# Optimization experiments

Measured on AMD Instinct MI355X. Metric: run time of the kernel, lower is better.

Reference implementation:

```python
import jax, jax.numpy as jnp
import numpy as np

B, H, C, HID, WIN, K = 8, 64, 128, 512, 4, 3
L = H * H

def _conv(x, w, groups, pad):
    return jax.lax.conv_general_dilated(
        x, w, (1, 1), [(pad, pad), (pad, pad)],
        dimension_numbers=('NCHW', 'OIHW', 'NCHW'), feature_group_count=groups)

def _ln(x, g, b):
    m = x.mean(-1, keepdims=True)
    v = ((x - m) ** 2).mean(-1, keepdims=True)
    return (x - m) * jax.lax.rsqrt(v + 1e-5) * g + b

def _gelu(x):
    return jax.nn.gelu(x, approximate=False)  # torch nn.GELU default = erf

def setup_inputs() -> dict:
    key = jax.random.key(0)
    ks = jax.random.split(key, 16)
    n = lambda i, sh: jax.random.normal(ks[i], sh, jnp.float32) * 0.02
    return dict(
        x=jax.random.normal(ks[0], (B, L, C), jnp.float32),
        ln1_g=jnp.ones((C,), jnp.float32), ln1_b=jnp.zeros((C,), jnp.float32),
        conv1_w=n(1, (WIN * C, C, K, K)),
        w_down=n(2, (WIN, C)), b_down=jnp.zeros((WIN,), jnp.float32),
        w1=n(3, (4 * WIN, WIN)), b1=jnp.zeros((4 * WIN,), jnp.float32),
        w2=n(4, (WIN, 4 * WIN)), b2=jnp.zeros((WIN,), jnp.float32),
        w_gk=n(5, (C, WIN * C)), b_gk=jnp.zeros((C,), jnp.float32),
        w_fus=n(6, (C, (WIN + 1) * C)), b_fus=jnp.zeros((C,), jnp.float32),
        ln2_g=jnp.ones((C,), jnp.float32), ln2_b=jnp.zeros((C,), jnp.float32),
        lin1_w=n(7, (HID, C)), lin1_b=jnp.zeros((HID,), jnp.float32),
        dw_w=n(8, (HID, 1, K, K)), dw_b=jnp.zeros((HID,), jnp.float32),
        lin2_w=n(9, (C, HID)), lin2_b=jnp.zeros((C,), jnp.float32),
    )

def _kernel_attn(x, conv1_w, w_down, b_down, w1, b1, w2, b2, w_gk, b_gk, w_fus, b_fus):
    ws = H // 2  # window grid is 2x2 since win_num=4
    xw = x.reshape(B, 2, ws, 2, ws, C).transpose(0, 1, 3, 5, 2, 4).reshape(B, WIN * C, ws, ws)
    wc = _conv(xw, conv1_w, WIN, 1)
    # WinKernel_Reweight (SE over windows)
    pooled = wc.mean((2, 3)).reshape(B, WIN, C)
    y = jnp.einsum('bgc,gc->bg', pooled, w_down) + b_down
    y = _gelu(y @ w1.T + b1)
    wgt = jax.nn.sigmoid(y @ w2.T + b2)
    k0 = conv1_w.reshape(WIN, C, C, K, K)
    kern = wgt[:, :, None, None, None, None] * k0[None]
    k_in = kern.transpose(0, 2, 1, 3, 4, 5).reshape(B * C, WIN * C, K, K)
    gk = jnp.einsum('om,nmij->noij', w_gk, k_in) + b_gk[None, :, None, None]
    kernels = jnp.concatenate([kern, gk.reshape(B, 1, C, C, K, K)], axis=1)
    kernels = kernels.reshape(B * (WIN + 1) * C, C, K, K)
    # per-sample dynamic grouped conv over full-resolution image
    ximg = x.reshape(B, H, H, C).transpose(0, 3, 1, 2)     # [B, C, H, W]
    xrep = jnp.tile(ximg, (1, WIN + 1, 1, 1)).reshape(1, B * (WIN + 1) * C, H, H)
    out = _conv(xrep, kernels, B * (WIN + 1), 1).reshape(B, (WIN + 1) * C, H, H)
    out = jnp.einsum('oc,bchw->bohw', w_fus, out) + b_fus[None, :, None, None]
    return out.transpose(0, 2, 3, 1).reshape(B, L, C)

def _leff(x, lin1_w, lin1_b, dw_w, dw_b, lin2_w, lin2_b):
    h = _gelu(x @ lin1_w.T + lin1_b)                       # [B, L, HID]
    h = h.reshape(B, H, H, HID).transpose(0, 3, 1, 2)
    h = _gelu(_conv(h, dw_w, HID, 1) + dw_b[None, :, None, None])  # depthwise 3x3
    h = h.transpose(0, 2, 3, 1).reshape(B, L, HID)
    return h @ lin2_w.T + lin2_b

def reference(x, ln1_g, ln1_b, conv1_w, w_down, b_down, w1, b1, w2, b2,
              w_gk, b_gk, w_fus, b_fus, ln2_g, ln2_b,
              lin1_w, lin1_b, dw_w, dw_b, lin2_w, lin2_b):
    x = x + _kernel_attn(_ln(x, ln1_g, ln1_b), conv1_w, w_down, b_down,
                         w1, b1, w2, b2, w_gk, b_gk, w_fus, b_fus)
    x = x + _leff(_ln(x, ln2_g, ln2_b), lin1_w, lin1_b, dw_w, dw_b, lin2_w, lin2_b)
    return x
```

## Files before the change

kernel.cpp:

```cpp
#include <hip/hip_runtime.h>
#include <math.h>

#define NB   8
#define HH   64
#define NC   128
#define NHID 512
#define NL   4096

typedef __attribute__((ext_vector_type(4))) float f32x4;
typedef __attribute__((ext_vector_type(8))) __bf16 bf16x8;

__device__ __forceinline__ float gelu_f(float v) {
  return 0.5f * v * (1.f + erff(v * 0.70710678118654752f));
}
__device__ __forceinline__ float sigmoid_f(float v) {
  return 1.f / (1.f + expf(-v));
}
__device__ __forceinline__ unsigned short f2bf(float f) {
  unsigned int u = __builtin_bit_cast(unsigned int, f);
  unsigned int r = (u + 0x7FFFu + ((u >> 16) & 1u)) >> 16;
  return (unsigned short)r;
}
__device__ __forceinline__ float bf2f(unsigned short h) {
  return __builtin_bit_cast(float, ((unsigned int)h) << 16);
}
__device__ __forceinline__ float bflo(unsigned int w) {
  return __builtin_bit_cast(float, w << 16);
}
__device__ __forceinline__ float bfhi(unsigned int w) {
  return __builtin_bit_cast(float, w & 0xFFFF0000u);
}
__device__ __forceinline__ void gld16(const void* g, void* l) {
  __builtin_amdgcn_global_load_lds(
      (const __attribute__((address_space(1))) unsigned int*)g,
      (__attribute__((address_space(3))) unsigned int*)l, 16, 0, 0);
}

template<bool SWZ>
__global__ __launch_bounds__(256) void ln_kernel(const float* __restrict__ x,
    const float* __restrict__ g, const float* __restrict__ bb, unsigned short* __restrict__ out) {
  int wv = threadIdx.x >> 6, l = threadIdx.x & 63;
  int row = blockIdx.x * 4 + wv;
  const float2 v = *(const float2*)(x + (size_t)row * NC + l * 2);
  float s = v.x + v.y, ss = v.x * v.x + v.y * v.y;
#pragma unroll
  for (int off = 32; off > 0; off >>= 1) {
    s  += __shfl_down(s, off);
    ss += __shfl_down(ss, off);
  }
  s = __shfl(s, 0); ss = __shfl(ss, 0);
  float mean = s * (1.f / NC);
  float rstd = rsqrtf(ss * (1.f / NC) - mean * mean + 1e-5f);
  const float2 gg = *(const float2*)(g + l * 2);
  const float2 bv = *(const float2*)(bb + l * 2);
  float o0 = (v.x - mean) * rstd * gg.x + bv.x;
  float o1 = (v.y - mean) * rstd * gg.y + bv.y;
  unsigned int pk = (unsigned int)f2bf(o0) | ((unsigned int)f2bf(o1) << 16);
  int c16 = l >> 2;
  int cs = SWZ ? (c16 ^ (row & 7)) : c16;
  *(unsigned int*)((char*)out + (size_t)row * 256 + (cs << 4) + (l & 3) * 4) = pk;
}

__global__ __launch_bounds__(128) void rs_kernel(const unsigned short* __restrict__ xln,
    float* __restrict__ RS) {
  int blk = blockIdx.x;
  int r = blk & 31, bw = blk >> 5;
  int win = bw & 3, b = bw >> 2;
  int hw = win >> 1, wn = win & 1;
  int cin = threadIdx.x;
  const unsigned short* base = xln + (((size_t)(b * 64 + hw * 32 + r)) * 64 + wn * 32) * NC + cin;
  float s = 0;
#pragma unroll
  for (int c = 0; c < 32; ++c) s += bf2f(base[(size_t)c * NC]);
  RS[(size_t)blk * 128 + cin] = s;
}

__global__ __launch_bounds__(128) void tfin_kernel(const unsigned short* __restrict__ xln,
    const float* __restrict__ RS, float* __restrict__ T) {
  int bw = blockIdx.x;
  int win = bw & 3, b = bw >> 2;
  int hw = win >> 1, wn = win & 1;
  int cin = threadIdx.x;
  const unsigned short* base = xln + (((size_t)(b * 64 + hw * 32)) * 64 + wn * 32) * NC + cin;
  float A = 0;
#pragma unroll
  for (int r = 0; r < 32; ++r) A += RS[(size_t)(bw * 32 + r) * 128 + cin];
  float r0  = RS[(size_t)(bw * 32) * 128 + cin];
  float r31 = RS[(size_t)(bw * 32 + 31) * 128 + cin];
  float c0 = 0, c31 = 0;
#pragma unroll
  for (int r = 0; r < 32; ++r) {
    c0  += bf2f(base[((size_t)r * 64) * NC]);
    c31 += bf2f(base[((size_t)r * 64 + 31) * NC]);
  }
  float x00 = bf2f(base[0]);
  float x0c = bf2f(base[(size_t)31 * NC]);
  float xr0 = bf2f(base[((size_t)31 * 64) * NC]);
  float xrc = bf2f(base[((size_t)31 * 64 + 31) * NC]);
  float* t = T + ((size_t)bw * 128 + cin) * 9;
  t[0] = A - r31 - c31 + xrc;
  t[1] = A - r31;
  t[2] = A - r31 - c0 + xr0;
  t[3] = A - c31;
  t[4] = A;
  t[5] = A - c0;
  t[6] = A - r0 - c31 + x0c;
  t[7] = A - r0;
  t[8] = A - r0 - c0 + x00;
}

__global__ __launch_bounds__(256) void se_kernel(const float* __restrict__ T,
    const float* __restrict__ U, const float* __restrict__ b_down,
    const float* __restrict__ w1, const float* __restrict__ b1,
    const float* __restrict__ w2, const float* __restrict__ b2, float* __restrict__ wgt) {
  __shared__ float ydot[32];
  int tid = threadIdx.x;
  int pair = tid >> 3, sub = tid & 7;
  int g = pair & 3;
  float acc = 0;
  const float* up = U + (size_t)g * 1152 + sub * 144;
  const float* tp = T + (size_t)pair * 1152 + sub * 144;
  for (int i = 0; i < 144; ++i) acc += up[i] * tp[i];
#pragma unroll
  for (int off = 4; off > 0; off >>= 1) acc += __shfl_down(acc, off);
  if (sub == 0) ydot[pair] = acc;
  __syncthreads();
  if (tid < NB) {
    int b = tid;
    float y[4];
#pragma unroll
    for (int gg = 0; gg < 4; ++gg) y[gg] = ydot[b * 4 + gg] * (1.f / 1024.f) + b_down[gg];
    float y1[16];
#pragma unroll
    for (int i = 0; i < 16; ++i) {
      float a = b1[i];
#pragma unroll
      for (int gg = 0; gg < 4; ++gg) a += y[gg] * w1[i * 4 + gg];
      y1[i] = gelu_f(a);
    }
#pragma unroll
    for (int gg = 0; gg < 4; ++gg) {
      float a = b2[gg];
#pragma unroll
      for (int i = 0; i < 16; ++i) a += y1[i] * w2[gg * 16 + i];
      wgt[b * 4 + gg] = sigmoid_f(a);
    }
  }
}

__global__ __launch_bounds__(128) void prep_ct_kernel(const float* __restrict__ conv1_w,
    unsigned short* __restrict__ ctp, unsigned short* __restrict__ ctq) {
  int oc = blockIdx.x;
  int w = oc >> 7, c = oc & 127;
  int t = threadIdx.x;
  float v[9];
#pragma unroll
  for (int j = 0; j < 9; ++j) v[j] = conv1_w[(size_t)oc * 1152 + t * 9 + j];
#pragma unroll
  for (int j = 0; j < 9; ++j) {
    unsigned short bv = f2bf(v[j]);
    size_t prow = (size_t)(w * 9 + j) * 128 + c;
    *(unsigned short*)((char*)ctp + prow * 256 + ((((t >> 3) ^ (c & 7)) << 4) + (t & 7) * 2)) = bv;
    size_t qrow = (size_t)(w * 9 + j) * 128 + t;
    *(unsigned short*)((char*)ctq + qrow * 256 + ((((c >> 3) ^ (t & 7)) << 4) + (c & 7) * 2)) = bv;
  }
}

__global__ __launch_bounds__(256) void prep_misc_kernel(
    const float* __restrict__ lin1_w, const float* __restrict__ lin2_w,
    const float* __restrict__ w_gk, const float* __restrict__ w_fus,
    const float* __restrict__ dw_w, const float* __restrict__ conv1_w,
    const float* __restrict__ w_down,
    unsigned short* __restrict__ w1o, unsigned short* __restrict__ w2o,
    unsigned short* __restrict__ wgko, unsigned short* __restrict__ wf1o,
    unsigned short* __restrict__ wf2o, float* __restrict__ dwt,
    float* __restrict__ U, float* __restrict__ sfus) {
  int blk = blockIdx.x, tid = threadIdx.x;
  if (blk < 32) {
    int idx = blk * 256 + tid;
    int n = idx >> 4, c16 = idx & 15;
    const float4 a = *(const float4*)(lin1_w + (size_t)n * 128 + c16 * 8);
    const float4 b = *(const float4*)(lin1_w + (size_t)n * 128 + c16 * 8 + 4);
    unsigned int p0 = (unsigned int)f2bf(a.x) | ((unsigned int)f2bf(a.y) << 16);
    unsigned int p1 = (unsigned int)f2bf(a.z) | ((unsigned int)f2bf(a.w) << 16);
    unsigned int p2 = (unsigned int)f2bf(b.x) | ((unsigned int)f2bf(b.y) << 16);
    unsigned int p3 = (unsigned int)f2bf(b.z) | ((unsigned int)f2bf(b.w) << 16);
    *(uint4*)((char*)w1o + (size_t)n * 256 + ((c16 ^ (n & 7)) << 4)) = make_uint4(p0, p1, p2, p3);
  } else if (blk < 64) {
    int idx = (blk - 32) * 256 + tid;
    int kt = idx >> 11, c = (idx >> 4) & 127, c16 = idx & 15;
    const float* s = lin2_w + (size_t)c * NHID + kt * 128 + c16 * 8;
    const float4 a = *(const float4*)(s);
    const float4 b = *(const float4*)(s + 4);
    unsigned int p0 = (unsigned int)f2bf(a.x) | ((unsigned int)f2bf(a.y) << 16);
    unsigned int p1 = (unsigned int)f2bf(a.z) | ((unsigned int)f2bf(a.w) << 16);
    unsigned int p2 = (unsigned int)f2bf(b.x) | ((unsigned int)f2bf(b.y) << 16);
    unsigned int p3 = (unsigned int)f2bf(b.z) | ((unsigned int)f2bf(b.w) << 16);
    *(uint4*)((char*)w2o + (size_t)(kt * 128 + c) * 256 + ((c16 ^ (c & 7)) << 4)) = make_uint4(p0, p1, p2, p3);
  } else if (blk < 96) {
    int idx = (blk - 64) * 256 + tid;
    int row = idx >> 4, c16 = idx & 15;
    int w = row >> 7, q = row & 127;
    const float* s = w_gk + (size_t)q * 512 + w * 128 + c16 * 8;
    const float4 a = *(const float4*)(s);
    const float4 b = *(const float4*)(s + 4);
    unsigned int p0 = (unsigned int)f2bf(a.x) | ((unsigned int)f2bf(a.y) << 16);
    unsigned int p1 = (unsigned int)f2bf(a.z) | ((unsigned int)f2bf(a.w) << 16);
    unsigned int p2 = (unsigned int)f2bf(b.x) | ((unsigned int)f2bf(b.y) << 16);
    unsigned int p3 = (unsigned int)f2bf(b.z) | ((unsigned int)f2bf(b.w) << 16);
    *(uint4*)((char*)wgko + (size_t)row * 256 + ((c16 ^ (row & 7)) << 4)) = make_uint4(p0, p1, p2, p3);
  } else if (blk < 136) {
    int idx = (blk - 96) * 256 + tid;
    if (idx < 8192) {
      int row = idx >> 4, c16 = idx & 15;
      int w = row >> 7, o = row & 127;
      const float* s = w_fus + (size_t)o * 640 + w * 128 + c16 * 8;
      const float4 a = *(const float4*)(s);
      const float4 b = *(const float4*)(s + 4);
      unsigned int p0 = (unsigned int)f2bf(a.x) | ((unsigned int)f2bf(a.y) << 16);
      unsigned int p1 = (unsigned int)f2bf(a.z) | ((unsigned int)f2bf(a.w) << 16);
      unsigned int p2 = (unsigned int)f2bf(b.x) | ((unsigned int)f2bf(b.y) << 16);
      unsigned int p3 = (unsigned int)f2bf(b.z) | ((unsigned int)f2bf(b.w) << 16);
      *(uint4*)((char*)wf1o + (size_t)row * 256 + ((c16 ^ (row & 7)) << 4)) = make_uint4(p0, p1, p2, p3);
    } else if (idx < 10240) {
      int i2 = idx - 8192;
      int row = i2 >> 4, c16 = i2 & 15;
      const float* s = w_fus + (size_t)row * 640 + 512 + c16 * 8;
      const float4 a = *(const float4*)(s);
      const float4 b = *(const float4*)(s + 4);
      unsigned int p0 = (unsigned int)f2bf(a.x) | ((unsigned int)f2bf(a.y) << 16);
      unsigned int p1 = (unsigned int)f2bf(a.z) | ((unsigned int)f2bf(a.w) << 16);
      unsigned int p2 = (unsigned int)f2bf(b.x) | ((unsigned int)f2bf(b.y) << 16);
      unsigned int p3 = (unsigned int)f2bf(b.z) | ((unsigned int)f2bf(b.w) << 16);
      *(uint4*)((char*)wf2o + (size_t)row * 256 + ((c16 ^ (row & 7)) << 4)) = make_uint4(p0, p1, p2, p3);
    }
  } else if (blk < 154) {
    int idx = (blk - 136) * 256 + tid;
    if (idx < 4608) {
      int p = idx / 1152, rem = idx - p * 1152;
      int tap = rem >> 7, c = rem & 127;
      dwt[idx] = dw_w[(size_t)(p * 128 + c) * 9 + tap];
    }
  } else if (blk < 172) {
    int idx = (blk - 154) * 256 + tid;
    if (idx < 4608) {
      int g = idx / 1152, rem = idx - g * 1152;
      float s = 0;
      for (int cout = 0; cout < 128; ++cout)
        s += w_down[g * 128 + cout] * conv1_w[(size_t)(g * 128 + cout) * 1152 + rem];
      U[idx] = s;
    }
  } else {
    if (tid < 128) {
      float s = 0;
      for (int p = 0; p < 128; ++p) s += w_fus[(size_t)tid * 640 + 512 + p];
      sfus[tid] = s;
    }
  }
}

__global__ __launch_bounds__(256) void gemmG_kernel(const unsigned short* __restrict__ Wgk,
    const unsigned short* __restrict__ CTP, unsigned short* __restrict__ Gbf) {
  __shared__ uint4 LA[2048];
  __shared__ uint4 LB[2048];
  int bx = blockIdx.x;
  int w = bx / 9;
  int tid = threadIdx.x, wv = tid >> 6, l = tid & 63;
  const char* ga = (const char*)Wgk + (size_t)w * 32768;
  const char* gb = (const char*)CTP + (size_t)bx * 32768;
  for (int i = wv; i < 32; i += 4) gld16(ga + (i << 10) + l * 16, (char*)LA + (i << 10));
  for (int i = wv; i < 32; i += 4) gld16(gb + (i << 10) + l * 16, (char*)LB + (i << 10));
  __syncthreads();
  const f32x4 zero = {0.f, 0.f, 0.f, 0.f};
  f32x4 acc[2][8];
#pragma unroll
  for (int mt = 0; mt < 2; ++mt)
#pragma unroll
    for (int nt = 0; nt < 8; ++nt) acc[mt][nt] = zero;
  bf16x8 af[2][4];
#pragma unroll
  for (int mt = 0; mt < 2; ++mt) {
    int r = wv * 16 + mt * 64 + (l & 15);
#pragma unroll
    for (int ks = 0; ks < 4; ++ks) {
      int c16 = ks * 4 + (l >> 4);
      af[mt][ks] = *(const bf16x8*)((const char*)LA + r * 256 + ((c16 ^ (r & 7)) << 4));
    }
  }
#pragma unroll
  for (int nt = 0; nt < 8; ++nt) {
    int n = nt * 16 + (l & 15);
    bf16x8 bq[4];
#pragma unroll
    for (int ks = 0; ks < 4; ++ks) {
      int c16 = ks * 4 + (l >> 4);
      bq[ks] = *(const bf16x8*)((const char*)LB + n * 256 + ((c16 ^ (n & 7)) << 4));
    }
#pragma unroll
    for (int ks = 0; ks < 4; ++ks)
#pragma unroll
      for (int mt = 0; mt < 2; ++mt)
        acc[mt][nt] = __builtin_amdgcn_mfma_f32_16x16x32_bf16(af[mt][ks], bq[ks], acc[mt][nt], 0, 0, 0);
  }
  char* gout = (char*)Gbf + (size_t)bx * 32768;
#pragma unroll
  for (int mt = 0; mt < 2; ++mt)
#pragma unroll
    for (int nt = 0; nt < 8; ++nt) {
      int p = nt * 16 + (l & 15);
#pragma unroll
      for (int r2 = 0; r2 < 4; ++r2) {
        int q = wv * 16 + mt * 64 + (l >> 4) * 4 + r2;
        *(unsigned short*)(gout + q * 256 + ((((p >> 3) ^ (q & 7)) << 4) + (p & 7) * 2)) =
            f2bf(acc[mt][nt][r2]);
      }
    }
}

__global__ __launch_bounds__(256) void gemmAW_kernel(const unsigned short* __restrict__ Wf1,
    const unsigned short* __restrict__ CTQ, const unsigned short* __restrict__ Wf2,
    const unsigned short* __restrict__ Gbf, float* __restrict__ AW) {
  __shared__ uint4 LA[2048];
  __shared__ uint4 LB[2048];
  int bx = blockIdx.x;
  int w = bx / 9;
  int tid = threadIdx.x, wv = tid >> 6, l = tid & 63;
  const f32x4 zero = {0.f, 0.f, 0.f, 0.f};
  f32x4 acc[2][8];
#pragma unroll
  for (int mt = 0; mt < 2; ++mt)
#pragma unroll
    for (int nt = 0; nt < 8; ++nt) acc[mt][nt] = zero;
  for (int ph = 0; ph < 2; ++ph) {
    if (ph) __syncthreads();
    const char* ga = ph ? (const char*)Wf2 : (const char*)Wf1 + (size_t)w * 32768;
    const char* gb = ph ? (const char*)Gbf + (size_t)bx * 32768
                        : (const char*)CTQ + (size_t)bx * 32768;
    for (int i = wv; i < 32; i += 4) gld16(ga + (i << 10) + l * 16, (char*)LA + (i << 10));
    for (int i = wv; i < 32; i += 4) gld16(gb + (i << 10) + l * 16, (char*)LB + (i << 10));
    __syncthreads();
    bf16x8 af[2][4];
#pragma unroll
    for (int mt = 0; mt < 2; ++mt) {
      int r = wv * 16 + mt * 64 + (l & 15);
#pragma unroll
      for (int ks = 0; ks < 4; ++ks) {
        int c16 = ks * 4 + (l >> 4);
        af[mt][ks] = *(const bf16x8*)((const char*)LA + r * 256 + ((c16 ^ (r & 7)) << 4));
      }
    }
#pragma unroll
    for (int nt = 0; nt < 8; ++nt) {
      int n = nt * 16 + (l & 15);
      bf16x8 bq[4];
#pragma unroll
      for (int ks = 0; ks < 4; ++ks) {
        int c16 = ks * 4 + (l >> 4);
        bq[ks] = *(const bf16x8*)((const char*)LB + n * 256 + ((c16 ^ (n & 7)) << 4));
      }
#pragma unroll
      for (int ks = 0; ks < 4; ++ks)
#pragma unroll
        for (int mt = 0; mt < 2; ++mt)
          acc[mt][nt] = __builtin_amdgcn_mfma_f32_16x16x32_bf16(af[mt][ks], bq[ks], acc[mt][nt], 0, 0, 0);
    }
  }
  float* aout = AW + (size_t)bx * 16384;
#pragma unroll
  for (int mt = 0; mt < 2; ++mt)
#pragma unroll
    for (int nt = 0; nt < 8; ++nt) {
      int q = nt * 16 + (l & 15);
#pragma unroll
      for (int r2 = 0; r2 < 4; ++r2) {
        int o = wv * 16 + mt * 64 + (l >> 4) * 4 + r2;
        aout[(size_t)o * 128 + q] = acc[mt][nt][r2];
      }
    }
}

__global__ __launch_bounds__(128) void m_kernel(const float* __restrict__ AW,
    const float* __restrict__ wgt, const float* __restrict__ sfus,
    const float* __restrict__ b_gk, unsigned short* __restrict__ Mb) {
  int blk = blockIdx.x;
  int b = blk >> 7;
  int o = blk & 127;
  int q = threadIdx.x;
  float a3 = sfus[o] * b_gk[q];
  float acc[9];
#pragma unroll
  for (int ij = 0; ij < 9; ++ij) acc[ij] = a3;
#pragma unroll
  for (int w = 0; w < 4; ++w) {
    float wv = wgt[b * 4 + w];
#pragma unroll
    for (int ij = 0; ij < 9; ++ij)
      acc[ij] += wv * AW[(((size_t)(w * 9 + ij) * 128 + o) * 128) + q];
  }
  int qswz = (q & 7) | (((q >> 3) ^ (o & 7)) << 3);
#pragma unroll
  for (int ij = 0; ij < 9; ++ij)
    Mb[(((size_t)(b * 9 + ij) * NC + o) * NC) + qswz] = f2bf(acc[ij]);
}

__global__ __launch_bounds__(256) void conv_kernel(const float* __restrict__ x0,
    const unsigned short* __restrict__ xln, const unsigned short* __restrict__ Mb,
    const float* __restrict__ b_fus, const float* __restrict__ ln2g,
    const float* __restrict__ ln2b, float* __restrict__ xout,
    unsigned short* __restrict__ xln2) {
  __shared__ uint4 XT[1600];
  __shared__ uint4 MT[2048];
  int bx = blockIdx.x;
  int b = bx >> 6, tile = bx & 63;
  int by = (tile >> 3) * 8, bxc = (tile & 7) * 8;
  int tid = threadIdx.x, wv = tid >> 6, l = tid & 63;
  for (int i = tid; i < 1600; i += 256) {
    int cell = i >> 4, c16 = i & 15;
    int pr = cell / 10, pc = cell - pr * 10;
    int gy = by + pr - 1, gx = bxc + pc - 1;
    uint4 v = make_uint4(0, 0, 0, 0);
    if ((unsigned)gy < 64u && (unsigned)gx < 64u)
      v = *(const uint4*)(xln + (((size_t)b * NL + gy * 64 + gx) * NC + c16 * 8));
    *(uint4*)((char*)XT + cell * 256 + ((c16 ^ (cell & 7)) << 4)) = v;
  }
  const char* mg = (const char*)Mb + (size_t)b * 9 * 32768;
  for (int i = wv; i < 32; i += 4) gld16(mg + (i << 10) + l * 16, (char*)MT + (i << 10));
  __syncthreads();

  const f32x4 zero = {0.f, 0.f, 0.f, 0.f};
  f32x4 acc[8];
#pragma unroll
  for (int nt = 0; nt < 8; ++nt) acc[nt] = zero;

  int sp = wv * 16 + (l & 15);
  int srow = sp >> 3, scol = sp & 7;

  for (int ij = 0; ij < 9; ++ij) {
    int di = ij / 3, dj = ij - di * 3;
    int cell = (srow + di) * 10 + scol + dj;
    bf16x8 af[4];
#pragma unroll
    for (int ks = 0; ks < 4; ++ks) {
      int c16 = ks * 4 + (l >> 4);
      af[ks] = *(const bf16x8*)((const char*)XT + cell * 256 + ((c16 ^ (cell & 7)) << 4));
    }
#pragma unroll
    for (int nt = 0; nt < 8; ++nt) {
      int oc = nt * 16 + (l & 15);
      bf16x8 bq[4];
#pragma unroll
      for (int ks = 0; ks < 4; ++ks) {
        int c16 = ks * 4 + (l >> 4);
        bq[ks] = *(const bf16x8*)((const char*)MT + oc * 256 + ((c16 ^ (oc & 7)) << 4));
      }
#pragma unroll
      for (int ks = 0; ks < 4; ++ks)
        acc[nt] = __builtin_amdgcn_mfma_f32_16x16x32_bf16(af[ks], bq[ks], acc[nt], 0, 0, 0);
    }
    __syncthreads();
    if (ij < 8) {
      const char* mg2 = mg + (size_t)(ij + 1) * 32768;
      for (int i = wv; i < 32; i += 4) gld16(mg2 + (i << 10) + l * 16, (char*)MT + (i << 10));
    }
    __syncthreads();
  }
  float s[4] = {0, 0, 0, 0}, ss2[4] = {0, 0, 0, 0};
  float vals[8][4];
#pragma unroll
  for (int nt = 0; nt < 8; ++nt) {
    int oc = nt * 16 + (l & 15);
    float bfv = b_fus[oc];
#pragma unroll
    for (int r2 = 0; r2 < 4; ++r2) {
      int sp2 = wv * 16 + (l >> 4) * 4 + r2;
      int gy = by + (sp2 >> 3), gx = bxc + (sp2 & 7);
      size_t gi = ((size_t)b * NL + gy * 64 + gx) * NC + oc;
      float v = x0[gi] + acc[nt][r2] + bfv;
      xout[gi] = v;
      vals[nt][r2] = v;
      s[r2] += v;
      ss2[r2] += v * v;
    }
  }
#pragma unroll
  for (int r2 = 0; r2 < 4; ++r2) {
#pragma unroll
    for (int off = 1; off < 16; off <<= 1) {
      s[r2]   += __shfl_xor(s[r2], off);
      ss2[r2] += __shfl_xor(ss2[r2], off);
    }
  }
  float mean[4], rstd[4];
#pragma unroll
  for (int r2 = 0; r2 < 4; ++r2) {
    mean[r2] = s[r2] * (1.f / 128.f);
    rstd[r2] = rsqrtf(ss2[r2] * (1.f / 128.f) - mean[r2] * mean[r2] + 1e-5f);
  }
#pragma unroll
  for (int nt = 0; nt < 8; ++nt) {
    int oc = nt * 16 + (l & 15);
    float gv = ln2g[oc], bv = ln2b[oc];
    int cc16 = oc >> 3, cby = (oc & 7) * 2;
#pragma unroll
    for (int r2 = 0; r2 < 4; ++r2) {
      int sp2 = wv * 16 + (l >> 4) * 4 + r2;
      int gy = by + (sp2 >> 3), gx = bxc + (sp2 & 7);
      size_t rowg = (size_t)b * NL + gy * 64 + gx;
      float o = (vals[nt][r2] - mean[r2]) * rstd[r2] * gv + bv;
      *(unsigned short*)((char*)xln2 + rowg * 256 + (((size_t)(cc16 ^ (int)(rowg & 7))) << 4) + cby) = f2bf(o);
    }
  }
}

__global__ __launch_bounds__(256) void lin1_kernel(const unsigned short* __restrict__ xa,
    const unsigned short* __restrict__ wb, const float* __restrict__ bias,
    unsigned short* __restrict__ h1p0, unsigned short* __restrict__ h1p123) {
  __shared__ uint4 XA[1024];
  __shared__ uint4 XB[2048];
  size_t rb = (size_t)blockIdx.x * 64;
  int tid = threadIdx.x, wv = tid >> 6, l = tid & 63;
  const char* ga = (const char*)xa + rb * 256;
  for (int i = wv; i < 16; i += 4) gld16(ga + (i << 10) + l * 16, (char*)XA + (i << 10));
  for (int i = wv; i < 32; i += 4) gld16((const char*)wb + (i << 10) + l * 16, (char*)XB + (i << 10));
  __syncthreads();
  int r = wv * 16 + (l & 15);
  bf16x8 af[4];
#pragma unroll
  for (int ks = 0; ks < 4; ++ks) {
    int c16 = ks * 4 + (l >> 4);
    af[ks] = *(const bf16x8*)((const char*)XA + r * 256 + ((c16 ^ (r & 7)) << 4));
  }
  const f32x4 zero = {0.f, 0.f, 0.f, 0.f};
  for (int cb = 0; cb < 4; ++cb) {
    f32x4 acc[8];
#pragma unroll
    for (int nt = 0; nt < 8; ++nt) acc[nt] = zero;
#pragma unroll
    for (int nt = 0; nt < 8; ++nt) {
      int n = nt * 16 + (l & 15);
      bf16x8 bq[4];
#pragma unroll
      for (int ks = 0; ks < 4; ++ks) {
        int c16 = ks * 4 + (l >> 4);
        bq[ks] = *(const bf16x8*)((const char*)XB + n * 256 + ((c16 ^ (n & 7)) << 4));
      }
#pragma unroll
      for (int ks = 0; ks < 4; ++ks)
        acc[nt] = __builtin_amdgcn_mfma_f32_16x16x32_bf16(af[ks], bq[ks], acc[nt], 0, 0, 0);
    }
    if (cb < 3) {
      __syncthreads();
      const char* gb = (const char*)wb + (size_t)(cb + 1) * 32768;
      for (int i = wv; i < 32; i += 4) gld16(gb + (i << 10) + l * 16, (char*)XB + (i << 10));
    }
    unsigned short* hp = (cb == 0) ? h1p0 : h1p123 + (size_t)(cb - 1) * 4194304;
#pragma unroll
    for (int nt = 0; nt < 8; ++nt) {
      int n = nt * 16 + (l & 15);
      float bsv = bias[cb * 128 + n];
#pragma unroll
      for (int r2 = 0; r2 < 4; ++r2) {
        size_t row = rb + wv * 16 + (l >> 4) * 4 + r2;
        hp[row * 128 + n] = f2bf(gelu_f(acc[nt][r2] + bsv));
      }
    }
    if (cb < 3) __syncthreads();
  }
}

__global__ __launch_bounds__(256) void dw_kernel(const unsigned short* __restrict__ h1p0,
    const unsigned short* __restrict__ h1p123, const float* __restrict__ dwt,
    const float* __restrict__ dw_b, unsigned short* __restrict__ h2p0,
    unsigned short* __restrict__ h2p123) {
  int bx = blockIdx.x;
  int cp = bx >> 8;
  int rem = bx & 255;
  int bimg = rem >> 5, ys = rem & 31;
  int p = cp >> 1, chh = cp & 1;
  int y0 = ys * 2;
  int tid = threadIdx.x;
  int grp = tid >> 3, c8 = tid & 7;
  int c16 = chh * 8 + c8;
  int x0 = grp * 2;
  const unsigned short* h1p = p ? h1p123 + (size_t)(p - 1) * 4194304 : h1p0;
  unsigned short* h2p = p ? h2p123 + (size_t)(p - 1) * 4194304 : h2p0;
  size_t ibase = (size_t)bimg * 4096;
  __shared__ float wsm[9][64];
  for (int i = tid; i < 576; i += 256)
    wsm[0][i] = dwt[(size_t)p * 1152 + (i >> 6) * 128 + chh * 64 + (i & 63)];
  int ch0 = p * 128 + c16 * 8;
  const float4 bs0 = *(const float4*)(dw_b + ch0);
  const float4 bs1 = *(const float4*)(dw_b + ch0 + 4);
  __syncthreads();

  const uint4 zero4 = make_uint4(0, 0, 0, 0);
  uint4 vA[4], vB[4], vC[4];

#define LOADROW(dst, yy) do {                                                     \
    int yv_ = (yy);                                                               \
    if ((unsigned)yv_ < 64u) {                                                    \
      _Pragma("unroll")                                                           \
      for (int xx = 0; xx < 4; ++xx) {                                            \
        int xp = x0 + xx - 1;                                                     \
        dst[xx] = ((unsigned)xp < 64u)                                            \
          ? *(const uint4*)(h1p + (ibase + (size_t)yv_ * 64 + xp) * 128 + c16 * 8)\
          : zero4;                                                                \
      }                                                                           \
    } else {                                                                      \
      _Pragma("unroll")                                                           \
      for (int xx = 0; xx < 4; ++xx) dst[xx] = zero4;                             \
    }                                                                             \
  } while (0)

#define DWROW(rm, rc, rp, yy) do {                                                \
    float acw[2][8];                                                              \
    _Pragma("unroll")                                                             \
    for (int r = 0; r < 2; ++r) {                                                 \
      acw[r][0] = bs0.x; acw[r][1] = bs0.y; acw[r][2] = bs0.z; acw[r][3] = bs0.w; \
      acw[r][4] = bs1.x; acw[r][5] = bs1.y; acw[r][6] = bs1.z; acw[r][7] = bs1.w; \
    }                                                                             \
    _Pragma("unroll")                                                             \
    for (int dx = 0; dx < 3; ++dx) {                                              \
      _Pragma("unroll")                                                           \
      for (int dy = 0; dy < 3; ++dy) {                                            \
        int tap = dy * 3 + dx;                                                    \
        const float4 wa = *(const float4*)(&wsm[tap][c8 * 8]);                    \
        const float4 wb2 = *(const float4*)(&wsm[tap][c8 * 8 + 4]);               \
        _Pragma("unroll")                                                         \
        for (int r = 0; r < 2; ++r) {                                             \
          const uint4 u = (dy == 0 ? rm : (dy == 1 ? rc : rp))[r + dx];           \
          acw[r][0] += wa.x * bflo(u.x);  acw[r][1] += wa.y * bfhi(u.x);          \
          acw[r][2] += wa.z * bflo(u.y);  acw[r][3] += wa.w * bfhi(u.y);          \
          acw[r][4] += wb2.x * bflo(u.z); acw[r][5] += wb2.y * bfhi(u.z);         \
          acw[r][6] += wb2.z * bflo(u.w); acw[r][7] += wb2.w * bfhi(u.w);         \
        }                                                                         \
      }                                                                           \
    }                                                                             \
    _Pragma("unroll")                                                             \
    for (int r = 0; r < 2; ++r) {                                                 \
      size_t sidx = ibase + (size_t)(yy) * 64 + x0 + r;                           \
      unsigned int o0 = (unsigned int)f2bf(gelu_f(acw[r][0])) | ((unsigned int)f2bf(gelu_f(acw[r][1])) << 16); \
      unsigned int o1 = (unsigned int)f2bf(gelu_f(acw[r][2])) | ((unsigned int)f2bf(gelu_f(acw[r][3])) << 16); \
      unsigned int o2 = (unsigned int)f2bf(gelu_f(acw[r][4])) | ((unsigned int)f2bf(gelu_f(acw[r][5])) << 16); \
      unsigned int o3 = (unsigned int)f2bf(gelu_f(acw[r][6])) | ((unsigned int)f2bf(gelu_f(acw[r][7])) << 16); \
      *(uint4*)(h2p + sidx * 128 + ((c16 ^ (int)(sidx & 7)) << 3)) = make_uint4(o0, o1, o2, o3); \
    }                                                                             \
  } while (0)

  LOADROW(vA, y0 - 1);
  LOADROW(vB, y0);
  LOADROW(vC, y0 + 1);
  DWROW(vA, vB, vC, y0);
  LOADROW(vA, y0 + 2);
  DWROW(vB, vC, vA, y0 + 1);
#undef LOADROW
#undef DWROW
}

__global__ __launch_bounds__(256) void lin2_kernel(const unsigned short* __restrict__ h2p0,
    const unsigned short* __restrict__ h2p123, const unsigned short* __restrict__ wb,
    const float* __restrict__ bias, const float* __restrict__ xres, float* __restrict__ out) {
  __shared__ uint4 XA[1024];
  __shared__ uint4 XB[2048];
  size_t rb = (size_t)blockIdx.x * 64;
  int tid = threadIdx.x, wv = tid >> 6, l = tid & 63;
  const f32x4 zero = {0.f, 0.f, 0.f, 0.f};
  f32x4 acc[8];
#pragma unroll
  for (int nt = 0; nt < 8; ++nt) acc[nt] = zero;
  int r = wv * 16 + (l & 15);
  for (int kt = 0; kt < 4; ++kt) {
    if (kt) __syncthreads();
    const unsigned short* hp = (kt == 0) ? h2p0 : h2p123 + (size_t)(kt - 1) * 4194304;
    const char* ga = (const char*)hp + rb * 256;
    const char* gb = (const char*)wb + (size_t)kt * 32768;
    for (int i = wv; i < 16; i += 4) gld16(ga + (i << 10) + l * 16, (char*)XA + (i << 10));
    for (int i = wv; i < 32; i += 4) gld16(gb + (i << 10) + l * 16, (char*)XB + (i << 10));
    __syncthreads();
    bf16x8 af[4];
#pragma unroll
    for (int ks = 0; ks < 4; ++ks) {
      int c16 = ks * 4 + (l >> 4);
      af[ks] = *(const bf16x8*)((const char*)XA + r * 256 + ((c16 ^ (r & 7)) << 4));
    }
#pragma unroll
    for (int nt = 0; nt < 8; ++nt) {
      int n = nt * 16 + (l & 15);
      bf16x8 bq[4];
#pragma unroll
      for (int ks = 0; ks < 4; ++ks) {
        int c16 = ks * 4 + (l >> 4);
        bq[ks] = *(const bf16x8*)((const char*)XB + n * 256 + ((c16 ^ (n & 7)) << 4));
      }
#pragma unroll
      for (int ks = 0; ks < 4; ++ks)
        acc[nt] = __builtin_amdgcn_mfma_f32_16x16x32_bf16(af[ks], bq[ks], acc[nt], 0, 0, 0);
    }
  }
#pragma unroll
  for (int nt = 0; nt < 8; ++nt) {
    int n = nt * 16 + (l & 15);
    float bsv = bias[n];
#pragma unroll
    for (int r2 = 0; r2 < 4; ++r2) {
      size_t row = rb + wv * 16 + (l >> 4) * 4 + r2;
      size_t gi = row * NC + n;
      out[gi] = xres[gi] + acc[nt][r2] + bsv;
    }
  }
}

extern "C" void kernel_launch(void* const* d_in, const int* in_sizes, int n_in,
                              void* d_out, int out_size, void* d_ws, size_t ws_size,
                              hipStream_t stream) {
  (void)in_sizes; (void)n_in; (void)out_size; (void)ws_size;
  const float* x       = (const float*)d_in[0];
  const float* ln1_g   = (const float*)d_in[1];
  const float* ln1_b   = (const float*)d_in[2];
  const float* conv1_w = (const float*)d_in[3];
  const float* w_down  = (const float*)d_in[4];
  const float* b_down  = (const float*)d_in[5];
  const float* w1      = (const float*)d_in[6];
  const float* b1      = (const float*)d_in[7];
  const float* w2      = (const float*)d_in[8];
  const float* b2      = (const float*)d_in[9];
  const float* w_gk    = (const float*)d_in[10];
  const float* b_gk    = (const float*)d_in[11];
  const float* w_fus   = (const float*)d_in[12];
  const float* b_fus   = (const float*)d_in[13];
  const float* ln2_g   = (const float*)d_in[14];
  const float* ln2_b   = (const float*)d_in[15];
  const float* lin1_w  = (const float*)d_in[16];
  const float* lin1_b  = (const float*)d_in[17];
  const float* dw_w    = (const float*)d_in[18];
  const float* dw_b    = (const float*)d_in[19];
  const float* lin2_w  = (const float*)d_in[20];
  const float* lin2_b  = (const float*)d_in[21];
  float* out = (float*)d_out;
  char* ws = (char*)d_ws;

  float*          xatt    = (float*)(ws);
  float*          Tb      = (float*)(ws + 16777216);
  float*          wgtb    = (float*)(ws + 16924672);
  float*          sfus    = (float*)(ws + 16925184);
  float*          dwt     = (float*)(ws + 16925696);
  unsigned short* Wgk_bf  = (unsigned short*)(ws + 16944128);
  unsigned short* Wf1_bf  = (unsigned short*)(ws + 17075200);
  unsigned short* Wf2_bf  = (unsigned short*)(ws + 17206272);
  unsigned short* w1_bf   = (unsigned short*)(ws + 17239040);
  unsigned short* w2_bf   = (unsigned short*)(ws + 17370112);
  unsigned short* M_bf    = (unsigned short*)(ws + 17501184);
  unsigned short* xln_bf  = (unsigned short*)(ws + 19860480);
  unsigned short* xln2_bf = (unsigned short*)(ws + 28249088);
  unsigned short* h1p123  = (unsigned short*)(ws + 36637696);
  unsigned short* h2p123  = (unsigned short*)(ws + 61803520);
  char* sc = ws + 28249088;
  float*          RSb     = (float*)(sc);
  float*          Ub      = (float*)(sc + 524288);
  unsigned short* CTP_bf  = (unsigned short*)(sc + 542720);
  unsigned short* CTQ_bf  = (unsigned short*)(sc + 1722368);
  unsigned short* G_bf    = (unsigned short*)(sc + 2902016);
  float*          AWb     = (float*)(sc + 4081664);

  ln_kernel<false><<<8192, 256, 0, stream>>>(x, ln1_g, ln1_b, xln_bf);
  prep_misc_kernel<<<173, 256, 0, stream>>>(lin1_w, lin2_w, w_gk, w_fus, dw_w, conv1_w, w_down,
                                            w1_bf, w2_bf, Wgk_bf, Wf1_bf, Wf2_bf, dwt, Ub, sfus);
  prep_ct_kernel<<<512, 128, 0, stream>>>(conv1_w, CTP_bf, CTQ_bf);
  rs_kernel<<<1024, 128, 0, stream>>>(xln_bf, RSb);
  tfin_kernel<<<32, 128, 0, stream>>>(xln_bf, RSb, Tb);
  se_kernel<<<1, 256, 0, stream>>>(Tb, Ub, b_down, w1, b1, w2, b2, wgtb);
  gemmG_kernel<<<36, 256, 0, stream>>>(Wgk_bf, CTP_bf, G_bf);
  gemmAW_kernel<<<36, 256, 0, stream>>>(Wf1_bf, CTQ_bf, Wf2_bf, G_bf, AWb);
  m_kernel<<<1024, 128, 0, stream>>>(AWb, wgtb, sfus, b_gk, M_bf);
  conv_kernel<<<512, 256, 0, stream>>>(x, xln_bf, M_bf, b_fus, ln2_g, ln2_b, xatt, xln2_bf);
  lin1_kernel<<<512, 256, 0, stream>>>(xln2_bf, w1_bf, lin1_b, xln_bf , h1p123);
  dw_kernel<<<2048, 256, 0, stream>>>(xln_bf , h1p123, dwt, dw_b,
                                      xln2_bf , h2p123);
  lin2_kernel<<<512, 256, 0, stream>>>(xln2_bf , h2p123, w2_bf, lin2_b, xatt, out);
}
```

Measured before the change: 165.8 us.

## Fuse SE weight projection into gemmG and split depthwise conv per row

The U projection (w_down times conv1 weights) moves out of a slow serial loop in prep_misc into gemmG, reusing the bf16 CTP tile already held in shared memory, and the se_kernel indexing changes to match the new U layout. The depthwise-conv kernel now handles one output row per block instead of two, doubling the grid for more parallelism. The cost is reloading three input rows per output row, and U is now computed from bf16-rounded weights, which slightly lowers its precision.

```diff
diff --git a/kernel.cpp b/kernel.cpp
--- a/kernel.cpp
+++ b/kernel.cpp
@@ -118,9 +118,13 @@
   int pair = tid >> 3, sub = tid & 7;
   int g = pair & 3;
   float acc = 0;
-  const float* up = U + (size_t)g * 1152 + sub * 144;
-  const float* tp = T + (size_t)pair * 1152 + sub * 144;
-  for (int i = 0; i < 144; ++i) acc += up[i] * tp[i];
+  for (int k = 0; k < 16; ++k) {
+    int cin = sub * 16 + k;
+    const float* tp = T + ((size_t)pair * 128 + cin) * 9;
+#pragma unroll
+    for (int ij = 0; ij < 9; ++ij)
+      acc += U[(size_t)(g * 9 + ij) * 128 + cin] * tp[ij];
+  }
 #pragma unroll
   for (int off = 4; off > 0; off >>= 1) acc += __shfl_down(acc, off);
   if (sub == 0) ydot[pair] = acc;
@@ -169,12 +173,11 @@
 __global__ __launch_bounds__(256) void prep_misc_kernel(
     const float* __restrict__ lin1_w, const float* __restrict__ lin2_w,
     const float* __restrict__ w_gk, const float* __restrict__ w_fus,
-    const float* __restrict__ dw_w, const float* __restrict__ conv1_w,
-    const float* __restrict__ w_down,
+    const float* __restrict__ dw_w,
     unsigned short* __restrict__ w1o, unsigned short* __restrict__ w2o,
     unsigned short* __restrict__ wgko, unsigned short* __restrict__ wf1o,
     unsigned short* __restrict__ wf2o, float* __restrict__ dwt,
-    float* __restrict__ U, float* __restrict__ sfus) {
+    float* __restrict__ sfus) {
   int blk = blockIdx.x, tid = threadIdx.x;
   if (blk < 32) {
     int idx = blk * 256 + tid;
@@ -241,15 +244,6 @@
       int tap = rem >> 7, c = rem & 127;
       dwt[idx] = dw_w[(size_t)(p * 128 + c) * 9 + tap];
     }
-  } else if (blk < 172) {
-    int idx = (blk - 154) * 256 + tid;
-    if (idx < 4608) {
-      int g = idx / 1152, rem = idx - g * 1152;
-      float s = 0;
-      for (int cout = 0; cout < 128; ++cout)
-        s += w_down[g * 128 + cout] * conv1_w[(size_t)(g * 128 + cout) * 1152 + rem];
-      U[idx] = s;
-    }
   } else {
     if (tid < 128) {
       float s = 0;
@@ -260,7 +254,8 @@
 }
 
 __global__ __launch_bounds__(256) void gemmG_kernel(const unsigned short* __restrict__ Wgk,
-    const unsigned short* __restrict__ CTP, unsigned short* __restrict__ Gbf) {
+    const unsigned short* __restrict__ CTP, const float* __restrict__ w_down,
+    unsigned short* __restrict__ Gbf, float* __restrict__ U) {
   __shared__ uint4 LA[2048];
   __shared__ uint4 LB[2048];
   int bx = blockIdx.x;
@@ -315,6 +310,17 @@
             f2bf(acc[mt][nt][r2]);
       }
     }
+  if (tid < 128) {
+    int cin = tid;
+    int hi = cin >> 3, lo = (cin & 7) * 2;
+    float s = 0;
+    for (int cout = 0; cout < 128; ++cout) {
+      unsigned short bv = *(const unsigned short*)((const char*)LB + cout * 256 +
+                                                   (((hi ^ (cout & 7)) << 4) + lo));
+      s += w_down[w * 128 + cout] * bf2f(bv);
+    }
+    U[(size_t)bx * 128 + cin] = s;
+  }
 }
 
 __global__ __launch_bounds__(256) void gemmAW_kernel(const unsigned short* __restrict__ Wf1,
@@ -573,11 +579,10 @@
     const float* __restrict__ dw_b, unsigned short* __restrict__ h2p0,
     unsigned short* __restrict__ h2p123) {
   int bx = blockIdx.x;
-  int cp = bx >> 8;
-  int rem = bx & 255;
-  int bimg = rem >> 5, ys = rem & 31;
+  int cp = bx >> 9;
+  int rem = bx & 511;
+  int bimg = rem >> 6, y = rem & 63;
   int p = cp >> 1, chh = cp & 1;
-  int y0 = ys * 2;
   int tid = threadIdx.x;
   int grp = tid >> 3, c8 = tid & 7;
   int c16 = chh * 8 + c8;
@@ -594,67 +599,50 @@
   __syncthreads();
 
   const uint4 zero4 = make_uint4(0, 0, 0, 0);
-  uint4 vA[4], vB[4], vC[4];
-
-#define LOADROW(dst, yy) do {                                                     \
-    int yv_ = (yy);                                                               \
-    if ((unsigned)yv_ < 64u) {                                                    \
-      _Pragma("unroll")                                                           \
-      for (int xx = 0; xx < 4; ++xx) {                                            \
-        int xp = x0 + xx - 1;                                                     \
-        dst[xx] = ((unsigned)xp < 64u)                                            \
-          ? *(const uint4*)(h1p + (ibase + (size_t)yv_ * 64 + xp) * 128 + c16 * 8)\
-          : zero4;                                                                \
-      }                                                                           \
-    } else {                                                                      \
-      _Pragma("unroll")                                                           \
-      for (int xx = 0; xx < 4; ++xx) dst[xx] = zero4;                             \
-    }                                                                             \
-  } while (0)
-
-#define DWROW(rm, rc, rp, yy) do {                                                \
-    float acw[2][8];                                                              \
-    _Pragma("unroll")                                                             \
-    for (int r = 0; r < 2; ++r) {                                                 \
-      acw[r][0] = bs0.x; acw[r][1] = bs0.y; acw[r][2] = bs0.z; acw[r][3] = bs0.w; \
-      acw[r][4] = bs1.x; acw[r][5] = bs1.y; acw[r][6] = bs1.z; acw[r][7] = bs1.w; \
-    }                                                                             \
-    _Pragma("unroll")                                                             \
-    for (int dx = 0; dx < 3; ++dx) {                                              \
-      _Pragma("unroll")                                                           \
-      for (int dy = 0; dy < 3; ++dy) {                                            \
-        int tap = dy * 3 + dx;                                                    \
-        const float4 wa = *(const float4*)(&wsm[tap][c8 * 8]);                    \
-        const float4 wb2 = *(const float4*)(&wsm[tap][c8 * 8 + 4]);               \
-        _Pragma("unroll")                                                         \
-        for (int r = 0; r < 2; ++r) {                                             \
-          const uint4 u = (dy == 0 ? rm : (dy == 1 ? rc : rp))[r + dx];           \
-          acw[r][0] += wa.x * bflo(u.x);  acw[r][1] += wa.y * bfhi(u.x);          \
-          acw[r][2] += wa.z * bflo(u.y);  acw[r][3] += wa.w * bfhi(u.y);          \
-          acw[r][4] += wb2.x * bflo(u.z); acw[r][5] += wb2.y * bfhi(u.z);         \
-          acw[r][6] += wb2.z * bflo(u.w); acw[r][7] += wb2.w * bfhi(u.w);         \
-        }                                                                         \
-      }                                                                           \
-    }                                                                             \
-    _Pragma("unroll")                                                             \
-    for (int r = 0; r < 2; ++r) {                                                 \
-      size_t sidx = ibase + (size_t)(yy) * 64 + x0 + r;                           \
-      unsigned int o0 = (unsigned int)f2bf(gelu_f(acw[r][0])) | ((unsigned int)f2bf(gelu_f(acw[r][1])) << 16); \
-      unsigned int o1 = (unsigned int)f2bf(gelu_f(acw[r][2])) | ((unsigned int)f2bf(gelu_f(acw[r][3])) << 16); \
-      unsigned int o2 = (unsigned int)f2bf(gelu_f(acw[r][4])) | ((unsigned int)f2bf(gelu_f(acw[r][5])) << 16); \
-      unsigned int o3 = (unsigned int)f2bf(gelu_f(acw[r][6])) | ((unsigned int)f2bf(gelu_f(acw[r][7])) << 16); \
-      *(uint4*)(h2p + sidx * 128 + ((c16 ^ (int)(sidx & 7)) << 3)) = make_uint4(o0, o1, o2, o3); \
-    }                                                                             \
-  } while (0)
-
-  LOADROW(vA, y0 - 1);
-  LOADROW(vB, y0);
-  LOADROW(vC, y0 + 1);
-  DWROW(vA, vB, vC, y0);
-  LOADROW(vA, y0 + 2);
-  DWROW(vB, vC, vA, y0 + 1);
-#undef LOADROW
-#undef DWROW
+  uint4 u[3][4];
+#pragma unroll
+  for (int dy = 0; dy < 3; ++dy) {
+    int yy = y + dy - 1;
+#pragma unroll
+    for (int xx = 0; xx < 4; ++xx) {
+      int xp = x0 + xx - 1;
+      bool ok = ((unsigned)yy < 64u) && ((unsigned)xp < 64u);
+      u[dy][xx] = ok ? *(const uint4*)(h1p + (ibase + (size_t)yy * 64 + xp) * 128 + c16 * 8)
+                     : zero4;
+    }
+  }
+  float acw[2][8];
+#pragma unroll
+  for (int r = 0; r < 2; ++r) {
+    acw[r][0] = bs0.x; acw[r][1] = bs0.y; acw[r][2] = bs0.z; acw[r][3] = bs0.w;
+    acw[r][4] = bs1.x; acw[r][5] = bs1.y; acw[r][6] = bs1.z; acw[r][7] = bs1.w;
+  }
+#pragma unroll
+  for (int dy = 0; dy < 3; ++dy) {
+#pragma unroll
+    for (int dx = 0; dx < 3; ++dx) {
+      int tap = dy * 3 + dx;
+      const float4 wa = *(const float4*)(&wsm[tap][c8 * 8 + chh * 0]);
+      const float4 wb2 = *(const float4*)(&wsm[tap][c8 * 8 + 4]);
+#pragma unroll
+      for (int r = 0; r < 2; ++r) {
+        const uint4 uu = u[dy][r + dx];
+        acw[r][0] += wa.x * bflo(uu.x);  acw[r][1] += wa.y * bfhi(uu.x);
+        acw[r][2] += wa.z * bflo(uu.y);  acw[r][3] += wa.w * bfhi(uu.y);
+        acw[r][4] += wb2.x * bflo(uu.z); acw[r][5] += wb2.y * bfhi(uu.z);
+        acw[r][6] += wb2.z * bflo(uu.w); acw[r][7] += wb2.w * bfhi(uu.w);
+      }
+    }
+  }
+#pragma unroll
+  for (int r = 0; r < 2; ++r) {
+    size_t sidx = ibase + (size_t)y * 64 + x0 + r;
+    unsigned int o0 = (unsigned int)f2bf(gelu_f(acw[r][0])) | ((unsigned int)f2bf(gelu_f(acw[r][1])) << 16);
+    unsigned int o1 = (unsigned int)f2bf(gelu_f(acw[r][2])) | ((unsigned int)f2bf(gelu_f(acw[r][3])) << 16);
+    unsigned int o2 = (unsigned int)f2bf(gelu_f(acw[r][4])) | ((unsigned int)f2bf(gelu_f(acw[r][5])) << 16);
+    unsigned int o3 = (unsigned int)f2bf(gelu_f(acw[r][6])) | ((unsigned int)f2bf(gelu_f(acw[r][7])) << 16);
+    *(uint4*)(h2p + sidx * 128 + ((c16 ^ (int)(sidx & 7)) << 3)) = make_uint4(o0, o1, o2, o3);
+  }
 }
 
 __global__ __launch_bounds__(256) void lin2_kernel(const unsigned short* __restrict__ h2p0,
@@ -763,18 +751,18 @@
   float*          AWb     = (float*)(sc + 4081664);
 
   ln_kernel<false><<<8192, 256, 0, stream>>>(x, ln1_g, ln1_b, xln_bf);
-  prep_misc_kernel<<<173, 256, 0, stream>>>(lin1_w, lin2_w, w_gk, w_fus, dw_w, conv1_w, w_down,
-                                            w1_bf, w2_bf, Wgk_bf, Wf1_bf, Wf2_bf, dwt, Ub, sfus);
+  prep_misc_kernel<<<155, 256, 0, stream>>>(lin1_w, lin2_w, w_gk, w_fus, dw_w,
+                                            w1_bf, w2_bf, Wgk_bf, Wf1_bf, Wf2_bf, dwt, sfus);
   prep_ct_kernel<<<512, 128, 0, stream>>>(conv1_w, CTP_bf, CTQ_bf);
   rs_kernel<<<1024, 128, 0, stream>>>(xln_bf, RSb);
+  gemmG_kernel<<<36, 256, 0, stream>>>(Wgk_bf, CTP_bf, w_down, G_bf, Ub);
   tfin_kernel<<<32, 128, 0, stream>>>(xln_bf, RSb, Tb);
   se_kernel<<<1, 256, 0, stream>>>(Tb, Ub, b_down, w1, b1, w2, b2, wgtb);
-  gemmG_kernel<<<36, 256, 0, stream>>>(Wgk_bf, CTP_bf, G_bf);
   gemmAW_kernel<<<36, 256, 0, stream>>>(Wf1_bf, CTQ_bf, Wf2_bf, G_bf, AWb);
   m_kernel<<<1024, 128, 0, stream>>>(AWb, wgtb, sfus, b_gk, M_bf);
   conv_kernel<<<512, 256, 0, stream>>>(x, xln_bf, M_bf, b_fus, ln2_g, ln2_b, xatt, xln2_bf);
   lin1_kernel<<<512, 256, 0, stream>>>(xln2_bf, w1_bf, lin1_b, xln_bf , h1p123);
-  dw_kernel<<<2048, 256, 0, stream>>>(xln_bf , h1p123, dwt, dw_b,
+  dw_kernel<<<4096, 256, 0, stream>>>(xln_bf , h1p123, dwt, dw_b,
                                       xln2_bf , h2p123);
   lin2_kernel<<<512, 256, 0, stream>>>(xln2_bf , h2p123, w2_bf, lin2_b, xatt, out);
 }
```

After: 188.5 us. +13.7%, slower.
